# Kernel tuning notes

Measured on AMD Instinct MI355X. Metric: run time of the kernel, lower is better.

## Reference

```python
import jax, jax.numpy as jnp
import numpy as np

SEQ_LEN = 1024
BATCH = 256
HIDDEN = 100
OUT = 1

L_FILTER = [-0.0106, 0.0329, 0.0308, -0.187, -0.028, 0.6309, 0.7148, 0.2304]
H_FILTER = [-0.2304, 0.7148, -0.6309, -0.028, 0.187, 0.0308, -0.0329, -0.0106]


def _create_W(P, is_l, rng):
    filt = L_FILTER if is_l else H_FILTER
    eps = np.min(np.abs(filt))
    W = rng.standard_normal((P, P)) * 0.1 * eps
    for i in range(P):
        for k, j in enumerate(range(i, min(i + len(filt), P))):
            W[i, j] = filt[k]
    return jnp.asarray(W, dtype=jnp.float32)


def setup_inputs() -> dict:
    key = jax.random.key(0)
    ks = jax.random.split(key, 16)
    rng = np.random.default_rng(0)
    T, H = SEQ_LEN, HIDDEN
    s = 1.0 / np.sqrt(H)

    def lstm_params(k):
        k1, k2, k3 = jax.random.split(k, 3)
        Wih = jax.random.uniform(k1, (4 * H, 1), jnp.float32, -s, s)
        Whh = jax.random.uniform(k2, (4 * H, H), jnp.float32, -s, s)
        b = jax.random.uniform(k3, (4 * H,), jnp.float32, -s, s)
        return Wih, Whh, b

    Wih1, Whh1, b1 = lstm_params(ks[0])
    Wih2, Whh2, b2 = lstm_params(ks[1])
    Wih3, Whh3, b3 = lstm_params(ks[2])
    return {
        "x": jax.random.normal(ks[3], (BATCH, T, 1), jnp.float32),
        "W1H": _create_W(T, False, rng),
        "b1H": jax.random.uniform(ks[4], (T,), jnp.float32, -1 / np.sqrt(T), 1 / np.sqrt(T)),
        "W1L": _create_W(T, True, rng),
        "b1L": jax.random.uniform(ks[5], (T,), jnp.float32, -1 / np.sqrt(T), 1 / np.sqrt(T)),
        "W2H": _create_W(T // 2, False, rng),
        "b2H": jax.random.uniform(ks[6], (T // 2,), jnp.float32, -1 / np.sqrt(T // 2), 1 / np.sqrt(T // 2)),
        "W2L": _create_W(T // 2, True, rng),
        "b2L": jax.random.uniform(ks[7], (T // 2,), jnp.float32, -1 / np.sqrt(T // 2), 1 / np.sqrt(T // 2)),
        "Wih1": Wih1, "Whh1": Whh1, "b1": b1,
        "Wih2": Wih2, "Whh2": Whh2, "b2": b2,
        "Wih3": Wih3, "Whh3": Whh3, "b3": b3,
        "Wout": jax.random.uniform(ks[8], (OUT, H), jnp.float32, -s, s),
        "bout": jax.random.uniform(ks[9], (OUT,), jnp.float32, -s, s),
    }


def _avgpool2(x):  # [B, L] -> [B, L//2], AvgPool1d(kernel=2, stride=2)
    B, L = x.shape
    return x.reshape(B, L // 2, 2).mean(-1)


def _lstm(x, Wih, Whh, b):
    # x: [B, T, 1]; torch LSTM gate order i, f, g, o; h0 = c0 = 0
    H = Whh.shape[1]
    gx = jnp.einsum('bti,gi->btg', x, Wih) + b  # [B, T, 4H]

    def step(carry, g):
        h, c = carry
        z = g + h @ Whh.T
        i, f, gg, o = jnp.split(z, 4, axis=-1)
        c = jax.nn.sigmoid(f) * c + jax.nn.sigmoid(i) * jnp.tanh(gg)
        h = jax.nn.sigmoid(o) * jnp.tanh(c)
        return (h, c), h

    B = x.shape[0]
    h0 = jnp.zeros((B, H), x.dtype)
    _, hs = jax.lax.scan(step, (h0, h0), jnp.swapaxes(gx, 0, 1))
    return jnp.swapaxes(hs, 0, 1)  # [B, T, H]


def reference(x, W1H, b1H, W1L, b1L, W2H, b2H, W2L, b2L,
              Wih1, Whh1, b1, Wih2, Whh2, b2, Wih3, Whh3, b3, Wout, bout):
    inp = x[:, :, -1]  # [B, T]
    ah1 = jax.nn.sigmoid(inp @ W1H.T + b1H)
    al1 = jax.nn.sigmoid(inp @ W1L.T + b1L)
    xh1 = _avgpool2(ah1)  # [B, T/2]
    xl1 = _avgpool2(al1)  # [B, T/2]
    ah2 = jax.nn.sigmoid(xl1 @ W2H.T + b2H)
    al2 = jax.nn.sigmoid(xl1 @ W2L.T + b2L)
    xh2 = _avgpool2(ah2)  # [B, T/4]
    xl2 = _avgpool2(al2)  # [B, T/4]
    s1 = _lstm(xh1[..., None], Wih1, Whh1, b1)
    s2 = _lstm(xh2[..., None], Wih2, Whh2, b2)
    s3 = _lstm(xl2[..., None], Wih3, Whh3, b3)
    cat = jnp.concatenate([s1, s2, s3], axis=1)  # [B, T, H]
    out = cat @ Wout.T + bout  # [B, T, OUT]
    return out[:, -1, :]
```

## Files before the change

kernel.cpp:

```cpp
#include <hip/hip_runtime.h>
#include <math.h>

typedef __bf16 bf16x8 __attribute__((ext_vector_type(8)));
typedef _Float16 f16x8 __attribute__((ext_vector_type(8)));
typedef float f32x4 __attribute__((ext_vector_type(4)));

__device__ __forceinline__ unsigned short f2bf(float f) {
  unsigned int u = __builtin_bit_cast(unsigned int, f);
  u += 0x7fffu + ((u >> 16) & 1u);
  return (unsigned short)(u >> 16);
}
__device__ __forceinline__ unsigned int pack2bf(float a, float b) {
  return (unsigned int)f2bf(a) | ((unsigned int)f2bf(b) << 16);
}

#define GK_PADK 40
template <int WFP32, int XFP32>
__global__ __launch_bounds__(256) void gemm_mfma_sig_pool(
    const void* __restrict__ Wv, const float* __restrict__ bias,
    const void* __restrict__ Xv, void* __restrict__ Y,
    int K, int Np, int out_bf16) {
  __shared__ unsigned short Wt[64][GK_PADK];
  __shared__ unsigned short Xt[64][GK_PADK];
  const int tid = threadIdx.x;
  const int i_base = blockIdx.x * 64;
  const int b_base = blockIdx.y * 64;
  const int srow = tid >> 2, sseg = tid & 3;
  const int wv = tid >> 6, lane = tid & 63;
  const int wn = wv & 1, wb = wv >> 1;
  const int L15 = lane & 15, q = lane >> 4;

  f32x4 acc[2][2] = {};
  for (int k0 = 0; k0 < K; k0 += 32) {
    if (WFP32) {
      const float* Wf = (const float*)Wv;
      const float4 a = *(const float4*)&Wf[(size_t)(i_base + srow) * K + k0 + sseg * 8];
      const float4 b = *(const float4*)&Wf[(size_t)(i_base + srow) * K + k0 + sseg * 8 + 4];
      uint4 p = { pack2bf(a.x, a.y), pack2bf(a.z, a.w), pack2bf(b.x, b.y), pack2bf(b.z, b.w) };
      *(uint4*)&Wt[srow][sseg * 8] = p;
    } else {
      *(uint4*)&Wt[srow][sseg * 8] =
          *(const uint4*)&((const unsigned short*)Wv)[(size_t)(i_base + srow) * K + k0 + sseg * 8];
    }
    if (XFP32) {
      const float* Xf = (const float*)Xv;
      const float4 a = *(const float4*)&Xf[(size_t)(b_base + srow) * K + k0 + sseg * 8];
      const float4 b = *(const float4*)&Xf[(size_t)(b_base + srow) * K + k0 + sseg * 8 + 4];
      uint4 p = { pack2bf(a.x, a.y), pack2bf(a.z, a.w), pack2bf(b.x, b.y), pack2bf(b.z, b.w) };
      *(uint4*)&Xt[srow][sseg * 8] = p;
    } else {
      *(uint4*)&Xt[srow][sseg * 8] =
          *(const uint4*)&((const unsigned short*)Xv)[(size_t)(b_base + srow) * K + k0 + sseg * 8];
    }
    __syncthreads();
    bf16x8 a0 = *(const bf16x8*)&Wt[wn * 32 + L15][q * 8];
    bf16x8 a1 = *(const bf16x8*)&Wt[wn * 32 + 16 + L15][q * 8];
    bf16x8 b0 = *(const bf16x8*)&Xt[wb * 32 + L15][q * 8];
    bf16x8 b1 = *(const bf16x8*)&Xt[wb * 32 + 16 + L15][q * 8];
    acc[0][0] = __builtin_amdgcn_mfma_f32_16x16x32_bf16(a0, b0, acc[0][0], 0, 0, 0);
    acc[0][1] = __builtin_amdgcn_mfma_f32_16x16x32_bf16(a0, b1, acc[0][1], 0, 0, 0);
    acc[1][0] = __builtin_amdgcn_mfma_f32_16x16x32_bf16(a1, b0, acc[1][0], 0, 0, 0);
    acc[1][1] = __builtin_amdgcn_mfma_f32_16x16x32_bf16(a1, b1, acc[1][1], 0, 0, 0);
    __syncthreads();
  }

  const int nb0 = i_base + wn * 32;
  const int bc0 = b_base + wb * 32 + L15;
#pragma unroll
  for (int mg = 0; mg < 2; mg++) {
    const int nrow = nb0 + mg * 16 + q * 4;
    const float bi0 = bias[nrow], bi1 = bias[nrow + 1];
    const float bi2 = bias[nrow + 2], bi3 = bias[nrow + 3];
#pragma unroll
    for (int bg = 0; bg < 2; bg++) {
      const int b = bc0 + bg * 16;
      f32x4 A = acc[mg][bg];
      const float a0 = __builtin_amdgcn_rcpf(1.f + __expf(-(A[0] + bi0)));
      const float a1 = __builtin_amdgcn_rcpf(1.f + __expf(-(A[1] + bi1)));
      const float a2 = __builtin_amdgcn_rcpf(1.f + __expf(-(A[2] + bi2)));
      const float a3 = __builtin_amdgcn_rcpf(1.f + __expf(-(A[3] + bi3)));
      const float p0 = 0.5f * (a0 + a1), p1 = 0.5f * (a2 + a3);
      const int pidx = nrow >> 1;
      if (out_bf16) {
        *(unsigned int*)&((unsigned short*)Y)[(size_t)b * Np + pidx] = pack2bf(p0, p1);
      } else {
        *(float2*)&((float*)Y)[(size_t)b * Np + pidx] = make_float2(p0, p1);
      }
    }
  }
}

__global__ __launch_bounds__(256) void prep_whh(
    const float* __restrict__ Whh, const float* __restrict__ b3,
    _Float16* __restrict__ P) {
  const int idx = blockIdx.x * 256 + threadIdx.x;
  if (idx >= 400 * 16) return;
  const int row = idx >> 4, ch = idx & 15;
  const int hid = row >> 2, gate = row & 3;
  const int src = gate * 100 + hid;
  f16x8 v;
#pragma unroll
  for (int j = 0; j < 8; j++) {
    const int k = ch * 8 + j;
    float f = 0.f;
    if (k < 100) f = Whh[(size_t)src * 100 + k];
    else if (k == 100) f = b3[src];
    v[j] = (_Float16)f;
  }
  *(f16x8*)&P[(size_t)row * 128 + ch * 8] = v;
}

#define TSTEPS 256

__global__ __launch_bounds__(512) void lstm_mfma(
    const float* __restrict__ X, const _Float16* __restrict__ P,
    const float* __restrict__ Wih, const float* __restrict__ Wout,
    const float* __restrict__ bout, float* __restrict__ out) {
  const int bat = blockIdx.x;
  const int t = threadIdx.x;
  const int w = t >> 6, lane = t & 63;
  const int quad = lane >> 4, c = lane & 15;
  const int TB = (w == 7) ? 21 : w * 3;
  const int NT = (w == 7) ? 4 : 3;

  __shared__ __align__(16) _Float16 hbuf[2][128];
  __shared__ float xrow[TSTEPS];
  __shared__ float red[128];

  for (int i = t; i < TSTEPS; i += 512) xrow[i] = X[(size_t)bat * TSTEPS + i];
  if (t < 128) { hbuf[0][t] = (_Float16)0.f; hbuf[1][t] = (_Float16)0.f; }
  __syncthreads();
  if (t < 2) hbuf[t][100] = (_Float16)1.f;

#define LDA(J, KT) const f16x8 A##J##KT = \
    *(const f16x8*)&P[(size_t)((TB + J) * 16 + c) * 128 + (KT) * 32 + quad * 8];
  LDA(0,0) LDA(0,1) LDA(0,2) LDA(0,3)
  LDA(1,0) LDA(1,1) LDA(1,2) LDA(1,3)
  LDA(2,0) LDA(2,1) LDA(2,2) LDA(2,3)
  LDA(3,0) LDA(3,1) LDA(3,2) LDA(3,3)
#undef LDA

  const bool act = (c < NT);
  const int myhid = 4 * (TB + (act ? c : 0)) + quad;
  const float u_i = Wih[0 * 100 + myhid];
  const float u_f = Wih[1 * 100 + myhid];
  const float u_g = Wih[2 * 100 + myhid];
  const float u_o = Wih[3 * 100 + myhid];
  float cst = 0.f;
  __syncthreads();

#define SIG(zz) __builtin_amdgcn_rcpf(1.f + __expf(-(zz)))
  for (int step = 0; step < TSTEPS; step++) {
    const int cur = step & 1, nxt = cur ^ 1;
    const _Float16* hc = hbuf[cur];
    const f16x8 B0 = *(const f16x8*)&hc[0 * 32 + quad * 8];
    const f16x8 B1 = *(const f16x8*)&hc[1 * 32 + quad * 8];
    const f16x8 B2 = *(const f16x8*)&hc[2 * 32 + quad * 8];
    const f16x8 B3 = *(const f16x8*)&hc[3 * 32 + quad * 8];

    f32x4 z0, z1, z2, z3 = {0.f, 0.f, 0.f, 0.f};
#define TILE(J, ZD)                                                          \
    {                                                                        \
      f32x4 za = {0.f, 0.f, 0.f, 0.f}, zb = za;                              \
      za = __builtin_amdgcn_mfma_f32_16x16x32_f16(A##J##0, B0, za, 0, 0, 0); \
      zb = __builtin_amdgcn_mfma_f32_16x16x32_f16(A##J##2, B2, zb, 0, 0, 0); \
      za = __builtin_amdgcn_mfma_f32_16x16x32_f16(A##J##1, B1, za, 0, 0, 0); \
      zb = __builtin_amdgcn_mfma_f32_16x16x32_f16(A##J##3, B3, zb, 0, 0, 0); \
      ZD = za + zb;                                                          \
    }
    TILE(0, z0)
    TILE(1, z1)
    TILE(2, z2)
    if (w == 7) TILE(3, z3)
#undef TILE

    const f32x4 zz = (c == 0) ? z0 : (c == 1) ? z1 : (c == 2) ? z2 : z3;
    if (act) {
      const float xt = xrow[step];
      const float ai = SIG(fmaf(u_i, xt, zz[0]));
      const float af = SIG(fmaf(u_f, xt, zz[1]));
      const float ag = 2.f * SIG(2.f * fmaf(u_g, xt, zz[2])) - 1.f;
      const float ao = SIG(fmaf(u_o, xt, zz[3]));
      cst = fmaf(af, cst, ai * ag);
      const float th = 2.f * SIG(2.f * cst) - 1.f;
      hbuf[nxt][myhid] = (_Float16)(ao * th);
    }
    __syncthreads();
  }
#undef SIG

  if (t < 128) {
    float a = 0.f;
    if (t < 100) a = (float)hbuf[0][t] * Wout[t];
    red[t] = a;
  }
  __syncthreads();
  if (t == 0) {
    float s = 0.f;
#pragma unroll
    for (int k = 0; k < 128; k++) s += red[k];
    out[bat] = s + bout[0];
  }
}

extern "C" void kernel_launch(void* const* d_in, const int* in_sizes, int n_in,
                              void* d_out, int out_size, void* d_ws, size_t ws_size,
                              hipStream_t stream) {
  const float* x    = (const float*)d_in[0];
  const float* W1L  = (const float*)d_in[3];
  const float* b1L  = (const float*)d_in[4];
  const float* W2L  = (const float*)d_in[7];
  const float* b2L  = (const float*)d_in[8];
  const float* Wih3 = (const float*)d_in[15];
  const float* Whh3 = (const float*)d_in[16];
  const float* b3   = (const float*)d_in[17];
  const float* Wout = (const float*)d_in[18];
  const float* bout = (const float*)d_in[19];
  float* out = (float*)d_out;

  unsigned short* xl1b = (unsigned short*)d_ws;
  float* xl2 = (float*)(xl1b + (size_t)256 * 512);
  _Float16* P = (_Float16*)(xl2 + (size_t)256 * 256);

  prep_whh<<<25, 256, 0, stream>>>(Whh3, b3, P);
  gemm_mfma_sig_pool<1, 1><<<dim3(16, 4), 256, 0, stream>>>(W1L, b1L, x, xl1b, 1024, 512, 1);
  gemm_mfma_sig_pool<1, 0><<<dim3(8, 4), 256, 0, stream>>>(W2L, b2L, xl1b, xl2, 512, 256, 0);
  lstm_mfma<<<256, 512, 0, stream>>>(xl2, P, Wih3, Wout, bout, out);
}
```

Before: 276.1 us.

## Trim LSTM K-tile to 96 and spread gate activations across lanes

The recurrent matmul now uses three K=32 MFMA tiles instead of four. The leftover four hidden columns (96..99) and the bias are added per lane in fp32 from global Whh, which drops a quarter of the MFMAs on the serial per-step critical path. Gate nonlinearities are distributed so each of four lanes computes one gate's sigmoid/tanh, and DPP broadcasts gather the four gate values, replacing four transcendental evaluations per thread. The loop is unrolled by two with fixed buffer pointers, and the launch bound asks for two blocks per CU, which may constrain registers.

```diff
diff --git a/kernel.cpp b/kernel.cpp
--- a/kernel.cpp
+++ b/kernel.cpp
@@ -3,6 +3,7 @@
 
 typedef __bf16 bf16x8 __attribute__((ext_vector_type(8)));
 typedef _Float16 f16x8 __attribute__((ext_vector_type(8)));
+typedef _Float16 f16x4 __attribute__((ext_vector_type(4)));
 typedef float f32x4 __attribute__((ext_vector_type(4)));
 
 __device__ __forceinline__ unsigned short f2bf(float f) {
@@ -104,7 +105,6 @@
     const int k = ch * 8 + j;
     float f = 0.f;
     if (k < 100) f = Whh[(size_t)src * 100 + k];
-    else if (k == 100) f = b3[src];
     v[j] = (_Float16)f;
   }
   *(f16x8*)&P[(size_t)row * 128 + ch * 8] = v;
@@ -112,9 +112,23 @@
 
 #define TSTEPS 256
 
-__global__ __launch_bounds__(512) void lstm_mfma(
+__device__ __forceinline__ float qb0(float x) {
+  return __builtin_bit_cast(float, __builtin_amdgcn_mov_dpp(__builtin_bit_cast(int, x), 0x00, 0xf, 0xf, true));
+}
+__device__ __forceinline__ float qb1(float x) {
+  return __builtin_bit_cast(float, __builtin_amdgcn_mov_dpp(__builtin_bit_cast(int, x), 0x55, 0xf, 0xf, true));
+}
+__device__ __forceinline__ float qb2(float x) {
+  return __builtin_bit_cast(float, __builtin_amdgcn_mov_dpp(__builtin_bit_cast(int, x), 0xAA, 0xf, 0xf, true));
+}
+__device__ __forceinline__ float qb3(float x) {
+  return __builtin_bit_cast(float, __builtin_amdgcn_mov_dpp(__builtin_bit_cast(int, x), 0xFF, 0xf, 0xf, true));
+}
+
+__global__ __launch_bounds__(512, 2) void lstm_mfma(
     const float* __restrict__ X, const _Float16* __restrict__ P,
-    const float* __restrict__ Wih, const float* __restrict__ Wout,
+    const float* __restrict__ Whh, const float* __restrict__ Wih,
+    const float* __restrict__ b3, const float* __restrict__ Wout,
     const float* __restrict__ bout, float* __restrict__ out) {
   const int bat = blockIdx.x;
   const int t = threadIdx.x;
@@ -129,64 +143,80 @@
 
   for (int i = t; i < TSTEPS; i += 512) xrow[i] = X[(size_t)bat * TSTEPS + i];
   if (t < 128) { hbuf[0][t] = (_Float16)0.f; hbuf[1][t] = (_Float16)0.f; }
-  __syncthreads();
-  if (t < 2) hbuf[t][100] = (_Float16)1.f;
 
 #define LDA(J, KT) const f16x8 A##J##KT = \
     *(const f16x8*)&P[(size_t)((TB + J) * 16 + c) * 128 + (KT) * 32 + quad * 8];
-  LDA(0,0) LDA(0,1) LDA(0,2) LDA(0,3)
-  LDA(1,0) LDA(1,1) LDA(1,2) LDA(1,3)
-  LDA(2,0) LDA(2,1) LDA(2,2) LDA(2,3)
-  LDA(3,0) LDA(3,1) LDA(3,2) LDA(3,3)
+  LDA(0,0) LDA(0,1) LDA(0,2)
+  LDA(1,0) LDA(1,1) LDA(1,2)
+  LDA(2,0) LDA(2,1) LDA(2,2)
+  LDA(3,0) LDA(3,1) LDA(3,2)
 #undef LDA
 
-  const bool act = (c < NT);
-  const int myhid = 4 * (TB + (act ? c : 0)) + quad;
-  const float u_i = Wih[0 * 100 + myhid];
-  const float u_f = Wih[1 * 100 + myhid];
-  const float u_g = Wih[2 * 100 + myhid];
-  const float u_o = Wih[3 * 100 + myhid];
+  const bool act = (c < 4 * NT);
+  const int J = c >> 2, g = c & 3;
+  const int myhid = 4 * (TB + (act ? J : 0)) + quad;
+  const int grow = g * 100 + myhid;
+  const float u_ = Wih[grow];
+  const float bz = b3[grow];
+  const float4 wt = *(const float4*)&Whh[(size_t)grow * 100 + 96];
+  const float kk = (g == 2) ? 2.f : 1.f;
+  const float mm = (g == 2) ? 2.f : 1.f;
+  const float dd = (g == 2) ? -1.f : 0.f;
   float cst = 0.f;
   __syncthreads();
 
 #define SIG(zz) __builtin_amdgcn_rcpf(1.f + __expf(-(zz)))
-  for (int step = 0; step < TSTEPS; step++) {
-    const int cur = step & 1, nxt = cur ^ 1;
-    const _Float16* hc = hbuf[cur];
-    const f16x8 B0 = *(const f16x8*)&hc[0 * 32 + quad * 8];
-    const f16x8 B1 = *(const f16x8*)&hc[1 * 32 + quad * 8];
-    const f16x8 B2 = *(const f16x8*)&hc[2 * 32 + quad * 8];
-    const f16x8 B3 = *(const f16x8*)&hc[3 * 32 + quad * 8];
-
-    f32x4 z0, z1, z2, z3 = {0.f, 0.f, 0.f, 0.f};
-#define TILE(J, ZD)                                                          \
-    {                                                                        \
-      f32x4 za = {0.f, 0.f, 0.f, 0.f}, zb = za;                              \
-      za = __builtin_amdgcn_mfma_f32_16x16x32_f16(A##J##0, B0, za, 0, 0, 0); \
-      zb = __builtin_amdgcn_mfma_f32_16x16x32_f16(A##J##2, B2, zb, 0, 0, 0); \
-      za = __builtin_amdgcn_mfma_f32_16x16x32_f16(A##J##1, B1, za, 0, 0, 0); \
-      zb = __builtin_amdgcn_mfma_f32_16x16x32_f16(A##J##3, B3, zb, 0, 0, 0); \
-      ZD = za + zb;                                                          \
-    }
-    TILE(0, z0)
-    TILE(1, z1)
-    TILE(2, z2)
-    if (w == 7) TILE(3, z3)
-#undef TILE
-
-    const f32x4 zz = (c == 0) ? z0 : (c == 1) ? z1 : (c == 2) ? z2 : z3;
-    if (act) {
-      const float xt = xrow[step];
-      const float ai = SIG(fmaf(u_i, xt, zz[0]));
-      const float af = SIG(fmaf(u_f, xt, zz[1]));
-      const float ag = 2.f * SIG(2.f * fmaf(u_g, xt, zz[2])) - 1.f;
-      const float ao = SIG(fmaf(u_o, xt, zz[3]));
-      cst = fmaf(af, cst, ai * ag);
-      const float th = 2.f * SIG(2.f * cst) - 1.f;
-      hbuf[nxt][myhid] = (_Float16)(ao * th);
-    }
-    __syncthreads();
-  }
+#define STEPB(HC, HN, XT)                                                      \
+  {                                                                            \
+    const _Float16* hc = (HC);                                                 \
+    const f16x8 B0 = *(const f16x8*)&hc[0 * 32 + quad * 8];                    \
+    const f16x8 B1 = *(const f16x8*)&hc[1 * 32 + quad * 8];                    \
+    const f16x8 B2 = *(const f16x8*)&hc[2 * 32 + quad * 8];                    \
+    f32x4 z0 = {0.f,0.f,0.f,0.f}, z1 = z0, z2 = z0, z3 = z0;                   \
+    { f32x4 za = z0, zb = z0;                                                  \
+      za = __builtin_amdgcn_mfma_f32_16x16x32_f16(A00, B0, za, 0, 0, 0);       \
+      zb = __builtin_amdgcn_mfma_f32_16x16x32_f16(A01, B1, zb, 0, 0, 0);       \
+      za = __builtin_amdgcn_mfma_f32_16x16x32_f16(A02, B2, za, 0, 0, 0);       \
+      z0 = za + zb; }                                                          \
+    { f32x4 za = {0.f,0.f,0.f,0.f}, zb = za;                                   \
+      za = __builtin_amdgcn_mfma_f32_16x16x32_f16(A10, B0, za, 0, 0, 0);       \
+      zb = __builtin_amdgcn_mfma_f32_16x16x32_f16(A11, B1, zb, 0, 0, 0);       \
+      za = __builtin_amdgcn_mfma_f32_16x16x32_f16(A12, B2, za, 0, 0, 0);       \
+      z1 = za + zb; }                                                          \
+    { f32x4 za = {0.f,0.f,0.f,0.f}, zb = za;                                   \
+      za = __builtin_amdgcn_mfma_f32_16x16x32_f16(A20, B0, za, 0, 0, 0);       \
+      zb = __builtin_amdgcn_mfma_f32_16x16x32_f16(A21, B1, zb, 0, 0, 0);       \
+      za = __builtin_amdgcn_mfma_f32_16x16x32_f16(A22, B2, za, 0, 0, 0);       \
+      z2 = za + zb; }                                                          \
+    if (w == 7) {                                                              \
+      f32x4 za = {0.f,0.f,0.f,0.f}, zb = za;                                   \
+      za = __builtin_amdgcn_mfma_f32_16x16x32_f16(A30, B0, za, 0, 0, 0);       \
+      zb = __builtin_amdgcn_mfma_f32_16x16x32_f16(A31, B1, zb, 0, 0, 0);       \
+      za = __builtin_amdgcn_mfma_f32_16x16x32_f16(A32, B2, za, 0, 0, 0);       \
+      z3 = za + zb; }                                                          \
+    if (act) {                                                                 \
+      const f32x4 zt = (J == 0) ? z0 : (J == 1) ? z1 : (J == 2) ? z2 : z3;     \
+      float zs = (g == 0) ? zt[0] : (g == 1) ? zt[1] : (g == 2) ? zt[2] : zt[3];\
+      const f16x4 ht = *(const f16x4*)&hc[96];                                 \
+      zs = fmaf(wt.x, (float)ht[0], zs);                                       \
+      zs = fmaf(wt.y, (float)ht[1], zs);                                       \
+      zs = fmaf(wt.z, (float)ht[2], zs);                                       \
+      zs = fmaf(wt.w, (float)ht[3], zs);                                       \
+      zs = fmaf(u_, (XT), zs + bz);                                            \
+      const float a = mm * SIG(kk * zs) + dd;                                  \
+      const float ai = qb0(a), af = qb1(a), ag = qb2(a), ao = qb3(a);          \
+      cst = fmaf(af, cst, ai * ag);                                            \
+      const float th = 2.f * SIG(2.f * cst) - 1.f;                             \
+      if (g == 0) (HN)[myhid] = (_Float16)(ao * th);                           \
+    }                                                                          \
+    __syncthreads();                                                           \
+  }
+
+  for (int step = 0; step < TSTEPS; step += 2) {
+    STEPB(hbuf[0], hbuf[1], xrow[step]);
+    STEPB(hbuf[1], hbuf[0], xrow[step + 1]);
+  }
+#undef STEPB
 #undef SIG
 
   if (t < 128) {
@@ -225,5 +255,5 @@
   prep_whh<<<25, 256, 0, stream>>>(Whh3, b3, P);
   gemm_mfma_sig_pool<1, 1><<<dim3(16, 4), 256, 0, stream>>>(W1L, b1L, x, xl1b, 1024, 512, 1);
   gemm_mfma_sig_pool<1, 0><<<dim3(8, 4), 256, 0, stream>>>(W2L, b2L, xl1b, xl2, 512, 256, 0);
-  lstm_mfma<<<256, 512, 0, stream>>>(xl2, P, Wih3, Wout, bout, out);
-}
+  lstm_mfma<<<256, 512, 0, stream>>>(xl2, P, Whh3, Wih3, b3, Wout, bout, out);
+}
```

Measured after the change: 264.6 us. 4.1% less time.
